# Performance work log

Measured on AMD Instinct MI355X. Metric: run time of the kernel, lower is better.

Reference implementation:

```python
import jax, jax.numpy as jnp
import numpy as np

B, S, D = 4, 4096, 512      # batch, seq_len, data_embedding_size
FH = 2048                    # forecasting_hidden_size
H = 64                       # lstm_hidden_size (proj_size=1 since H>1)


def setup_inputs() -> dict:
    key = jax.random.key(0)
    ks = jax.random.split(key, 10)
    sD, sFH, sH = 1.0 / np.sqrt(D), 1.0 / np.sqrt(FH), 1.0 / np.sqrt(H)
    return {
        "x": jax.random.normal(ks[0], (B, S, D), dtype=jnp.float32),
        # forecasting head: Linear(D->FH) then Linear(FH->D)
        "W1": jax.random.uniform(ks[1], (FH, D), minval=-sD, maxval=sD),
        "b1": jax.random.uniform(ks[2], (FH,), minval=-sD, maxval=sD),
        "W2": jax.random.uniform(ks[3], (D, FH), minval=-sFH, maxval=sFH),
        "b2": jax.random.uniform(ks[4], (D,), minval=-sFH, maxval=sFH),
        # LSTM (1 layer, proj_size=1): gate order i,f,g,o
        "Wih": jax.random.uniform(ks[5], (4 * H, D), minval=-sH, maxval=sH),
        "Whh": jax.random.uniform(ks[6], (4 * H, 1), minval=-sH, maxval=sH),  # recurrent input is projected h (size 1)
        "bih": jax.random.uniform(ks[7], (4 * H,), minval=-sH, maxval=sH),
        "bhh": jax.random.uniform(ks[8], (4 * H,), minval=-sH, maxval=sH),
        "Whr": jax.random.uniform(ks[9], (1, H), minval=-sH, maxval=sH),  # projection h_inner -> h
    }


def reference(x, W1, b1, W2, b2, Wih, Whh, bih, bhh, Whr):
    Bx, Sx, Dx = x.shape
    flat = x.reshape(-1, Dx)                       # [B*S, D]
    fore = (flat @ W1.T + b1) @ W2.T + b2          # [B*S, D]  (two linears, no activation)

    # Original code loops i in range(S) over the FLATTENED sequence -> only first S tokens.
    xs = flat[:Sx]
    fs = fore[:Sx]

    def cell(h, c, inp):
        # gates = W_ih x + b_ih + W_hh h + b_hh ; PyTorch order i,f,g,o
        g = Wih @ inp + bih + Whh @ h + bhh        # [4H]
        i, f, gg, o = jnp.split(g, 4)
        c2 = jax.nn.sigmoid(f) * c + jax.nn.sigmoid(i) * jnp.tanh(gg)
        h2 = Whr @ (jax.nn.sigmoid(o) * jnp.tanh(c2))   # projected hidden, shape [1]
        return h2, c2

    def step(carry, tok):
        h, c = carry
        xt, ft = tok
        h2, c2 = cell(h, c, xt)        # real token: updates state
        hf, _ = cell(h2, c2, ft)       # forecasted token: peeks, does not update state
        return (h2, c2), (h2[0], hf[0])

    init = (jnp.zeros((1,), x.dtype), jnp.zeros((H,), x.dtype))
    _, (p, pf) = jax.lax.scan(step, init, (xs, fs))   # p, pf: [S]

    progress = jnp.broadcast_to(p[None, :], (Bx, Sx))
    forecasted_progress = jnp.broadcast_to(pf[None, :], (Bx, Sx))
    return progress, forecasted_progress, fore.reshape(1, -1, Dx)
```

## Files before the change

### kernel.cpp

```cpp
#include <hip/hip_runtime.h>
#include <hip/hip_bf16.h>


#if __has_builtin(__builtin_amdgcn_exp2f)
__device__ __forceinline__ float EXP2(float x) { return __builtin_amdgcn_exp2f(x); }
#else
__device__ __forceinline__ float EXP2(float x) { return __expf(x * 0.6931471805599453f); }
#endif
#if __has_builtin(__builtin_amdgcn_rcpf)
__device__ __forceinline__ float RCPF(float x) { return __builtin_amdgcn_rcpf(x); }
#else
__device__ __forceinline__ float RCPF(float x) { return 1.0f / x; }
#endif

constexpr float L2E  = 1.4426950408889634f;
constexpr float L2E2 = 2.8853900817779268f;

__device__ __forceinline__ float sig_f(float x)  { return RCPF(1.0f + EXP2(-L2E * x)); }
__device__ __forceinline__ float tanh_f(float x) { return fmaf(-2.0f, RCPF(1.0f + EXP2(L2E2 * x)), 1.0f); }

template<int CTRL>
__device__ __forceinline__ float dppadd(float x) {
    return x + __int_as_float(__builtin_amdgcn_update_dpp(
        0, __float_as_int(x), CTRL, 0xf, 0xf, true));
}
__device__ __forceinline__ float dpp_sum64_lane63(float x) {
    x = dppadd<0x111>(x); x = dppadd<0x112>(x); x = dppadd<0x114>(x);
    x = dppadd<0x118>(x); x = dppadd<0x142>(x); x = dppadd<0x143>(x);
    return x;
}
__device__ __forceinline__ float readlane63(float x) {
    return __int_as_float(__builtin_amdgcn_readlane(__float_as_int(x), 63));
}
__device__ __forceinline__ float readlane_s(float x, int s) {
    return __int_as_float(__builtin_amdgcn_readlane(__float_as_int(x), s));
}

using bf16x8 = __attribute__((ext_vector_type(8))) __bf16;
using f32x4  = __attribute__((ext_vector_type(4))) float;

__device__ __forceinline__ void mfma_tile128_lds(
    const __hip_bfloat16* __restrict__ A, int lda,
    const __hip_bfloat16* __restrict__ B, int ldb,
    int K, int bm, int bn,
    const float* __restrict__ bias,
    float* __restrict__ Cf, int ldc,
    __hip_bfloat16* __restrict__ Cb,
    __hip_bfloat16* __restrict__ Ct, int ldt,
    __hip_bfloat16* __restrict__ Bs)
{
    const int tid  = threadIdx.x;
    const int w    = tid >> 6;
    const int lane = tid & 63;
    const int rc   = lane & 15;
    const int kg   = lane >> 4;
    const __hip_bfloat16* ap0 = A + (size_t)(bm + w * 16 + rc) * lda + kg * 8;
    const __hip_bfloat16* ap1 = ap0 + (size_t)64 * lda;

#define LD8(P) (*reinterpret_cast<const bf16x8*>(P))
    const f32x4 z{0.f, 0.f, 0.f, 0.f};
    f32x4 c00 = z, c01 = z, c02 = z, c03 = z;
    f32x4 c10 = z, c11 = z, c12 = z, c13 = z;

    for (int kb = 0; kb < K; kb += 512) {
        __syncthreads();
        #pragma unroll
        for (int i = 0; i < 16; ++i) {
            const int G = i * 256 + tid;
            const int row = G >> 6, kc = G & 63;
            const bf16x8 v = LD8(B + (size_t)(bn + row) * ldb + kb + kc * 8);
            *reinterpret_cast<bf16x8*>(Bs + row * 512 + ((kc ^ (row & 7)) << 3)) = v;
        }
        __syncthreads();

        bf16x8 a0 = LD8(ap0 + kb), a1 = LD8(ap1 + kb);
        #pragma unroll 4
        for (int s = 0; s < 16; ++s) {
            bf16x8 a0n = a0, a1n = a1;
            if (s < 15) {
                a0n = LD8(ap0 + kb + (s + 1) * 32);
                a1n = LD8(ap1 + kb + (s + 1) * 32);
            }
            bf16x8 bf[4];
            #pragma unroll
            for (int g = 0; g < 4; ++g) {
                const int row = g * 16 + rc;
                const int off = row * 512 + (((s * 4 + kg) ^ (row & 7)) << 3);
                bf[g] = *reinterpret_cast<const bf16x8*>(Bs + off);
            }
            c00 = __builtin_amdgcn_mfma_f32_16x16x32_bf16(a0, bf[0], c00, 0, 0, 0);
            c01 = __builtin_amdgcn_mfma_f32_16x16x32_bf16(a0, bf[1], c01, 0, 0, 0);
            c02 = __builtin_amdgcn_mfma_f32_16x16x32_bf16(a0, bf[2], c02, 0, 0, 0);
            c03 = __builtin_amdgcn_mfma_f32_16x16x32_bf16(a0, bf[3], c03, 0, 0, 0);
            c10 = __builtin_amdgcn_mfma_f32_16x16x32_bf16(a1, bf[0], c10, 0, 0, 0);
            c11 = __builtin_amdgcn_mfma_f32_16x16x32_bf16(a1, bf[1], c11, 0, 0, 0);
            c12 = __builtin_amdgcn_mfma_f32_16x16x32_bf16(a1, bf[2], c12, 0, 0, 0);
            c13 = __builtin_amdgcn_mfma_f32_16x16x32_bf16(a1, bf[3], c13, 0, 0, 0);
            a0 = a0n; a1 = a1n;
        }
    }
#undef LD8

    const int row0 = bm + w * 16 + kg * 4;
    const int colb = bn + rc;
#define EPI(ACC, HOFF, CT) {                                                  \
        const int col = colb + (CT) * 16;                                     \
        const float bb = bias ? bias[col] : 0.0f;                             \
        _Pragma("unroll")                                                     \
        for (int i = 0; i < 4; ++i) {                                         \
            const float v = (ACC)[i] + bb;                                    \
            const int row = row0 + (HOFF) + i;                                \
            if (Cf) Cf[(size_t)row * ldc + col] = v;                          \
            if (Cb) Cb[(size_t)row * ldc + col] = __float2bfloat16(v);        \
            if (Ct) Ct[(size_t)col * ldt + row] = __float2bfloat16(v);        \
        }}
    EPI(c00, 0, 0)  EPI(c01, 0, 1)  EPI(c02, 0, 2)  EPI(c03, 0, 3)
    EPI(c10, 64, 0) EPI(c11, 64, 1) EPI(c12, 64, 2) EPI(c13, 64, 3)
#undef EPI
}

__global__ __launch_bounds__(256) void conv_kernel(
    const float* __restrict__ x, const float* __restrict__ W2,
    const float* __restrict__ W1, const float* __restrict__ Wih,
    const float* __restrict__ bih, const float* __restrict__ bhh,
    __hip_bfloat16* __restrict__ xb, __hip_bfloat16* __restrict__ W2b,
    __hip_bfloat16* __restrict__ Wihb, __hip_bfloat16* __restrict__ W1t,
    float* __restrict__ gxbias)
{
    const int bid = blockIdx.x, tid = threadIdx.x;
#define CVT4(SRC, DST, BASE) {                                                \
        const size_t i = ((size_t)(BASE) * 256 + tid) * 4;                    \
        const float4 v = *reinterpret_cast<const float4*>((SRC) + i);         \
        __hip_bfloat16 o[4] = {__float2bfloat16(v.x), __float2bfloat16(v.y),  \
                               __float2bfloat16(v.z), __float2bfloat16(v.w)}; \
        *reinterpret_cast<ushort4*>((DST) + i) =                              \
            *reinterpret_cast<const ushort4*>(o); }
    if (bid < 8192) {
        CVT4(x, xb, bid)
    } else if (bid < 9216) {
        CVT4(W2, W2b, bid - 8192)
    } else if (bid < 9344) {
        CVT4(Wih, Wihb, bid - 9216)
    } else if (bid < 9600) {
        __shared__ float lds[64][65];
        const int b = bid - 9344;
        const int br = b >> 3, bc = b & 7;
        const int r0 = tid >> 4, c4 = (tid & 15) * 4;
        #pragma unroll
        for (int u = 0; u < 4; ++u) {
            const int row = r0 + u * 16;
            const float4 v = *reinterpret_cast<const float4*>(
                &W1[(size_t)(br * 64 + row) * 512 + bc * 64 + c4]);
            lds[row][c4 + 0] = v.x; lds[row][c4 + 1] = v.y;
            lds[row][c4 + 2] = v.z; lds[row][c4 + 3] = v.w;
        }
        __syncthreads();
        const int jj0 = tid >> 4, kk4 = (tid & 15) * 4;
        #pragma unroll
        for (int u = 0; u < 4; ++u) {
            const int jj = jj0 + u * 16;
            __hip_bfloat16 o[4] = {
                __float2bfloat16(lds[kk4 + 0][jj]), __float2bfloat16(lds[kk4 + 1][jj]),
                __float2bfloat16(lds[kk4 + 2][jj]), __float2bfloat16(lds[kk4 + 3][jj])};
            *reinterpret_cast<ushort4*>(
                &W1t[(size_t)(bc * 64 + jj) * 2048 + br * 64 + kk4]) =
                *reinterpret_cast<const ushort4*>(o);
        }
    } else {
        gxbias[tid] = bih[tid] + bhh[tid];
    }
#undef CVT4
}

__global__ __launch_bounds__(256) void prep_kernel(
    const float* __restrict__ W2, const float* __restrict__ b1,
    const float* __restrict__ b2,
    const __hip_bfloat16* __restrict__ W2b, const __hip_bfloat16* __restrict__ W1t,
    const __hip_bfloat16* __restrict__ xb, const __hip_bfloat16* __restrict__ Wihb,
    const float* __restrict__ gxbias,
    __hip_bfloat16* __restrict__ Weffb, __hip_bfloat16* __restrict__ WeffTb,
    float* __restrict__ beff, float* __restrict__ Gx)
{
    __shared__ __hip_bfloat16 Bs[64 * 512];
    const int bid = blockIdx.x;
    if (bid < 32) {
        const int bm = (bid >> 3) * 128, bn = (bid & 7) * 64;
        mfma_tile128_lds(W2b, 2048, W1t, 2048, 2048, bm, bn, nullptr,
                         nullptr, 512, Weffb, WeffTb, 512, Bs);
    } else if (bid < 40) {
        const int w = threadIdx.x >> 6, j = threadIdx.x & 63;
        const int base = (bid - 32) * 64 + w * 16;
        for (int o = 0; o < 16; ++o) {
            const int i = base + o;
            float s = 0.0f;
            #pragma unroll
            for (int m = 0; m < 32; ++m)
                s = fmaf(W2[(size_t)i * 2048 + j + 64 * m], b1[j + 64 * m], s);
            s = dpp_sum64_lane63(s);
            if (j == 63) beff[i] = s + b2[i];
        }
    } else {
        const int b = bid - 40;
        const int bm = (b >> 2) * 128, bn = (b & 3) * 64;
        mfma_tile128_lds(xb, 512, Wihb, 512, 512, bm, bn, gxbias,
                         Gx, 256, nullptr, nullptr, 0, Bs);
    }
}

__global__ __launch_bounds__(256) void fused_kernel(
    int phase, int first, int last,
    int fore_cnt, int gf_cnt, int wg_cnt,
    const __hip_bfloat16* __restrict__ xb, const __hip_bfloat16* __restrict__ Weffb,
    const __hip_bfloat16* __restrict__ WeffTb, const __hip_bfloat16* __restrict__ Wihb,
    __hip_bfloat16* __restrict__ Wgb, const __hip_bfloat16* __restrict__ Wgb_in,
    const float* __restrict__ Wih, const float* __restrict__ beff,
    float* __restrict__ bf2_out, const float* __restrict__ bf2,
    const float* __restrict__ Gx, float* __restrict__ Gf,
    const float* __restrict__ Gf_in, const float* __restrict__ gxbias,
    const float* __restrict__ Whh, const float* __restrict__ Whr,
    const float* __restrict__ hprev, float* __restrict__ hnext,
    float* __restrict__ P, float* __restrict__ Q,
    float* __restrict__ fore, float* __restrict__ out)
{
    __shared__ __hip_bfloat16 Bs[64 * 512];
    constexpr int CH = 32;
    constexpr int S = 4096, BS = 4 * 4096;

    if (blockIdx.x < 32) {
        const int chunk = blockIdx.x * 4 + (threadIdx.x >> 6);
        const int j = threadIdx.x & 63;
        const float wi = Whh[j], wf = Whh[64 + j];
        const float wg2 = Whh[128 + j], wo = Whh[192 + j];
        const float* ab = Gx + (size_t)chunk * CH * 256 + j;

        float hp = 0.0f;
        if (!first) {
            const int idx = chunk * CH - 1 + j;
            hp = (idx >= 0 && idx < S) ? hprev[idx] : 0.0f;
        }

        if (phase == 0) {
            float Pv = 1.0f, Qv = 0.0f;
            #pragma unroll 8
            for (int s = 0; s < CH; ++s) {
                const float hs = first ? 0.0f : readlane_s(hp, s);
                const float ai = ab[s * 256]       + wi  * hs;
                const float af = ab[s * 256 + 64]  + wf  * hs;
                const float ag = ab[s * 256 + 128] + wg2 * hs;
                const float si = sig_f(ai);
                const float sf = sig_f(af);
                const float tg = tanh_f(ag);
                Pv = sf * Pv;
                Qv = fmaf(sf, Qv, si * tg);
            }
            P[chunk * 64 + j] = Pv;
            Q[chunk * 64 + j] = Qv;
        } else {
            const float whr = Whr[j];
            float c = 0.0f;
            #pragma unroll 8
            for (int m = 0; m < chunk; ++m)
                c = fmaf(P[m * 64 + j], c, Q[m * 64 + j]);
            float vp = 0.0f, vpf = 0.0f;
            const float* gfp = Gf_in ? Gf_in + (size_t)chunk * CH * 256 + j : nullptr;
            const float bi0 = gxbias[j],        bi1 = gxbias[64 + j];
            const float bi2 = gxbias[128 + j],  bi3 = gxbias[192 + j];
            #pragma unroll 4
            for (int s = 0; s < CH; ++s) {
                const float hs = first ? 0.0f : readlane_s(hp, s);
                const float ai = ab[s * 256]       + wi  * hs;
                const float af = ab[s * 256 + 64]  + wf  * hs;
                const float ag = ab[s * 256 + 128] + wg2 * hs;
                const float ao = ab[s * 256 + 192] + wo  * hs;
                const float si = sig_f(ai);
                const float sf = sig_f(af);
                const float tg = tanh_f(ag);
                const float so = sig_f(ao);
                c = fmaf(sf, c, si * tg);
                const float tc = tanh_f(c);
                float hv = tc * (so * whr);
                hv = dpp_sum64_lane63(hv);
                const float hn = readlane63(hv);
                vp = (j == s) ? hn : vp;
                if (last) {
                    const float fi = gfp[s * 256]       + bi0 + wi  * hn;
                    const float ff = gfp[s * 256 + 64]  + bi1 + wf  * hn;
                    const float fg = gfp[s * 256 + 128] + bi2 + wg2 * hn;
                    const float fo = gfp[s * 256 + 192] + bi3 + wo  * hn;
                    const float cf = sig_f(ff) * c + sig_f(fi) * tanh_f(fg);
                    float hf = sig_f(fo) * tanh_f(cf) * whr;
                    hf = dpp_sum64_lane63(hf);
                    const float hfn = readlane63(hf);
                    vpf = (j == s) ? hfn : vpf;
                }
            }
            if (j < CH) {
                const int t = chunk * CH + j;
                if (last) {
                    #pragma unroll
                    for (int b = 0; b < 4; ++b) {
                        out[b * S + t]      = vp;
                        out[BS + b * S + t] = vpf;
                    }
                } else {
                    hnext[t] = vp;
                }
            }
        }
        return;
    }

    const int bt = blockIdx.x - 32;
    if (bt < fore_cnt) {
        const int bm = (bt >> 3) * 128, bn = (bt & 7) * 64;
        mfma_tile128_lds(xb, 512, Weffb, 512, 512, bm, bn, beff,
                         fore, 512, nullptr, nullptr, 0, Bs);
    } else if (bt < fore_cnt + gf_cnt) {
        const int g = bt - fore_cnt;
        const int bm = (g >> 2) * 128, bn = (g & 3) * 64;
        mfma_tile128_lds(xb, 512, Wgb_in, 512, 512, bm, bn, bf2,
                         Gf, 256, nullptr, nullptr, 0, Bs);
    } else if (bt < fore_cnt + gf_cnt + wg_cnt) {
        const int t = bt - fore_cnt - gf_cnt;
        if (t < 16) {
            const int bm = (t >> 3) * 128, bn = (t & 7) * 64;
            mfma_tile128_lds(Wihb, 512, WeffTb, 512, 512, bm, bn, nullptr,
                             nullptr, 512, Wgb, nullptr, 0, Bs);
        } else {
            const int w = threadIdx.x >> 6, j = threadIdx.x & 63;
            for (int o = 0; o < 64; ++o) {
                const int i = w * 64 + o;
                float s = 0.0f;
                #pragma unroll
                for (int m = 0; m < 8; ++m)
                    s = fmaf(Wih[(size_t)i * 512 + j + 64 * m], beff[j + 64 * m], s);
                s = dpp_sum64_lane63(s);
                if (j == 63) bf2_out[i] = s;
            }
        }
    }
}

extern "C" void kernel_launch(void* const* d_in, const int* in_sizes, int n_in,
                              void* d_out, int out_size, void* d_ws, size_t ws_size,
                              hipStream_t stream) {
    const float* x   = (const float*)d_in[0];
    const float* W1  = (const float*)d_in[1];
    const float* b1  = (const float*)d_in[2];
    const float* W2  = (const float*)d_in[3];
    const float* b2  = (const float*)d_in[4];
    const float* Wih = (const float*)d_in[5];
    const float* Whh = (const float*)d_in[6];
    const float* bih = (const float*)d_in[7];
    const float* bhh = (const float*)d_in[8];
    const float* Whr = (const float*)d_in[9];
    float* out = (float*)d_out;

    constexpr int Bb = 4, S = 4096;
    const int M = Bb * S;

    float* ws      = (float*)d_ws;
    float* beff    = ws;
    float* gxbias  = beff + 512;
    float* bf2     = gxbias + 256;
    float* Gx      = bf2 + 256;
    float* Gf      = Gx + S * 256;
    float* Pp      = Gf + S * 256;
    float* Qq      = Pp + 8192;
    float* h0      = Qq + 8192;
    float* h1      = h0 + S;
    __hip_bfloat16* xb     = (__hip_bfloat16*)(h1 + S);
    __hip_bfloat16* W2b    = xb + (size_t)M * 512;
    __hip_bfloat16* W1t    = W2b + 512 * 2048;
    __hip_bfloat16* Wihb   = W1t + 512 * 2048;
    __hip_bfloat16* Weffb  = Wihb + 256 * 512;
    __hip_bfloat16* WeffTb = Weffb + 512 * 512;
    __hip_bfloat16* Wgb    = WeffTb + 512 * 512;

    float* fore = out + 2 * M;

    conv_kernel<<<9601, 256, 0, stream>>>(
        x, W2, W1, Wih, bih, bhh, xb, W2b, Wihb, W1t, gxbias);

    prep_kernel<<<168, 256, 0, stream>>>(
        W2, b1, b2, W2b, W1t, xb, Wihb, gxbias, Weffb, WeffTb, beff, Gx);

    fused_kernel<<<32 + 1024 + 17, 256, 0, stream>>>(
        0, 1, 0, 1024, 0, 17,
        xb, Weffb, WeffTb, Wihb, Wgb, Wgb, Wih, beff, bf2, bf2,
        Gx, Gf, nullptr, gxbias, Whh, Whr,
        h0, h0, Pp, Qq, fore, out);

    fused_kernel<<<32 + 128, 256, 0, stream>>>(
        1, 1, 0, 0, 128, 0,
        xb, Weffb, WeffTb, Wihb, Wgb, Wgb, Wih, beff, bf2, bf2,
        Gx, Gf, nullptr, gxbias, Whh, Whr,
        h0, h0, Pp, Qq, fore, out);

    fused_kernel<<<32, 256, 0, stream>>>(
        0, 0, 0, 0, 0, 0,
        xb, Weffb, WeffTb, Wihb, Wgb, Wgb, Wih, beff, bf2, bf2,
        Gx, Gf, nullptr, gxbias, Whh, Whr,
        h0, h1, Pp, Qq, fore, out);

    fused_kernel<<<32, 256, 0, stream>>>(
        1, 0, 1, 0, 0, 0,
        xb, Weffb, WeffTb, Wihb, Wgb, Wgb, Wih, beff, bf2, bf2,
        Gx, Gf, Gf, gxbias, Whh, Whr,
        h0, h1, Pp, Qq, fore, out);
}
```

Baseline: 154.7 us.

## Reschedule prep stages: overlap x conversion with Weff GEMM, split Wg/Gx kernel

```diff
diff --git a/kernel.cpp b/kernel.cpp
--- a/kernel.cpp
+++ b/kernel.cpp
@@ -119,13 +119,12 @@
 #undef EPI
 }
 
-__global__ __launch_bounds__(256) void conv_kernel(
-    const float* __restrict__ x, const float* __restrict__ W2,
-    const float* __restrict__ W1, const float* __restrict__ Wih,
+__global__ __launch_bounds__(256) void convA_kernel(
+    const float* __restrict__ W2, const float* __restrict__ W1,
+    const float* __restrict__ Wih,
     const float* __restrict__ bih, const float* __restrict__ bhh,
-    __hip_bfloat16* __restrict__ xb, __hip_bfloat16* __restrict__ W2b,
-    __hip_bfloat16* __restrict__ Wihb, __hip_bfloat16* __restrict__ W1t,
-    float* __restrict__ gxbias)
+    __hip_bfloat16* __restrict__ W2b, __hip_bfloat16* __restrict__ W1t,
+    __hip_bfloat16* __restrict__ Wihb, float* __restrict__ gxbias)
 {
     const int bid = blockIdx.x, tid = threadIdx.x;
 #define CVT4(SRC, DST, BASE) {                                                \
@@ -135,15 +134,11 @@
                                __float2bfloat16(v.z), __float2bfloat16(v.w)}; \
         *reinterpret_cast<ushort4*>((DST) + i) =                              \
             *reinterpret_cast<const ushort4*>(o); }
-    if (bid < 8192) {
-        CVT4(x, xb, bid)
-    } else if (bid < 9216) {
-        CVT4(W2, W2b, bid - 8192)
-    } else if (bid < 9344) {
-        CVT4(Wih, Wihb, bid - 9216)
-    } else if (bid < 9600) {
+    if (bid < 1024) {
+        CVT4(W2, W2b, bid)
+    } else if (bid < 1280) {
         __shared__ float lds[64][65];
-        const int b = bid - 9344;
+        const int b = bid - 1024;
         const int br = b >> 3, bc = b & 7;
         const int r0 = tid >> 4, c4 = (tid & 15) * 4;
         #pragma unroll
@@ -166,29 +161,30 @@
                 &W1t[(size_t)(bc * 64 + jj) * 2048 + br * 64 + kk4]) =
                 *reinterpret_cast<const ushort4*>(o);
         }
+    } else if (bid < 1408) {
+        CVT4(Wih, Wihb, bid - 1280)
     } else {
         gxbias[tid] = bih[tid] + bhh[tid];
     }
 #undef CVT4
 }
 
-__global__ __launch_bounds__(256) void prep_kernel(
-    const float* __restrict__ W2, const float* __restrict__ b1,
-    const float* __restrict__ b2,
+__global__ __launch_bounds__(256) void convB_kernel(
+    const float* __restrict__ x, const float* __restrict__ W2,
+    const float* __restrict__ b1, const float* __restrict__ b2,
     const __hip_bfloat16* __restrict__ W2b, const __hip_bfloat16* __restrict__ W1t,
-    const __hip_bfloat16* __restrict__ xb, const __hip_bfloat16* __restrict__ Wihb,
-    const float* __restrict__ gxbias,
+    __hip_bfloat16* __restrict__ xb,
     __hip_bfloat16* __restrict__ Weffb, __hip_bfloat16* __restrict__ WeffTb,
-    float* __restrict__ beff, float* __restrict__ Gx)
+    float* __restrict__ beff)
 {
     __shared__ __hip_bfloat16 Bs[64 * 512];
-    const int bid = blockIdx.x;
+    const int bid = blockIdx.x, tid = threadIdx.x;
     if (bid < 32) {
         const int bm = (bid >> 3) * 128, bn = (bid & 7) * 64;
         mfma_tile128_lds(W2b, 2048, W1t, 2048, 2048, bm, bn, nullptr,
                          nullptr, 512, Weffb, WeffTb, 512, Bs);
     } else if (bid < 40) {
-        const int w = threadIdx.x >> 6, j = threadIdx.x & 63;
+        const int w = tid >> 6, j = tid & 63;
         const int base = (bid - 32) * 64 + w * 16;
         for (int o = 0; o < 16; ++o) {
             const int i = base + o;
@@ -201,6 +197,47 @@
         }
     } else {
         const int b = bid - 40;
+        const float4* src = reinterpret_cast<const float4*>(x) + (size_t)b * 1024;
+        ushort4* dst = reinterpret_cast<ushort4*>(xb) + (size_t)b * 1024;
+        float4 v[4];
+        #pragma unroll
+        for (int u = 0; u < 4; ++u) v[u] = src[u * 256 + tid];
+        #pragma unroll
+        for (int u = 0; u < 4; ++u) {
+            __hip_bfloat16 o[4] = {__float2bfloat16(v[u].x), __float2bfloat16(v[u].y),
+                                   __float2bfloat16(v[u].z), __float2bfloat16(v[u].w)};
+            dst[u * 256 + tid] = *reinterpret_cast<const ushort4*>(o);
+        }
+    }
+}
+
+__global__ __launch_bounds__(256) void wggx_kernel(
+    const __hip_bfloat16* __restrict__ Wihb, const __hip_bfloat16* __restrict__ WeffTb,
+    const __hip_bfloat16* __restrict__ xb,
+    const float* __restrict__ Wih, const float* __restrict__ beff,
+    const float* __restrict__ gxbias,
+    __hip_bfloat16* __restrict__ Wgb, float* __restrict__ bf2,
+    float* __restrict__ Gx)
+{
+    __shared__ __hip_bfloat16 Bs[64 * 512];
+    const int bid = blockIdx.x;
+    if (bid < 16) {
+        const int bm = (bid >> 3) * 128, bn = (bid & 7) * 64;
+        mfma_tile128_lds(Wihb, 512, WeffTb, 512, 512, bm, bn, nullptr,
+                         nullptr, 512, Wgb, nullptr, 0, Bs);
+    } else if (bid == 16) {
+        const int w = threadIdx.x >> 6, j = threadIdx.x & 63;
+        for (int o = 0; o < 64; ++o) {
+            const int i = w * 64 + o;
+            float s = 0.0f;
+            #pragma unroll
+            for (int m = 0; m < 8; ++m)
+                s = fmaf(Wih[(size_t)i * 512 + j + 64 * m], beff[j + 64 * m], s);
+            s = dpp_sum64_lane63(s);
+            if (j == 63) bf2[i] = s;
+        }
+    } else {
+        const int b = bid - 17;
         const int bm = (b >> 2) * 128, bn = (b & 3) * 64;
         mfma_tile128_lds(xb, 512, Wihb, 512, 512, bm, bn, gxbias,
                          Gx, 256, nullptr, nullptr, 0, Bs);
@@ -209,12 +246,10 @@
 
 __global__ __launch_bounds__(256) void fused_kernel(
     int phase, int first, int last,
-    int fore_cnt, int gf_cnt, int wg_cnt,
+    int fore_cnt, int gf_cnt,
     const __hip_bfloat16* __restrict__ xb, const __hip_bfloat16* __restrict__ Weffb,
-    const __hip_bfloat16* __restrict__ WeffTb, const __hip_bfloat16* __restrict__ Wihb,
-    __hip_bfloat16* __restrict__ Wgb, const __hip_bfloat16* __restrict__ Wgb_in,
-    const float* __restrict__ Wih, const float* __restrict__ beff,
-    float* __restrict__ bf2_out, const float* __restrict__ bf2,
+    const __hip_bfloat16* __restrict__ Wgb_in,
+    const float* __restrict__ beff, const float* __restrict__ bf2,
     const float* __restrict__ Gx, float* __restrict__ Gf,
     const float* __restrict__ Gf_in, const float* __restrict__ gxbias,
     const float* __restrict__ Whh, const float* __restrict__ Whr,
@@ -312,7 +347,8 @@
 
     const int bt = blockIdx.x - 32;
     if (bt < fore_cnt) {
-        const int bm = (bt >> 3) * 128, bn = (bt & 7) * 64;
+        const int tile = (bt & 7) * 128 + (bt >> 3);
+        const int bm = (tile >> 3) * 128, bn = (tile & 7) * 64;
         mfma_tile128_lds(xb, 512, Weffb, 512, 512, bm, bn, beff,
                          fore, 512, nullptr, nullptr, 0, Bs);
     } else if (bt < fore_cnt + gf_cnt) {
@@ -320,24 +356,6 @@
         const int bm = (g >> 2) * 128, bn = (g & 3) * 64;
         mfma_tile128_lds(xb, 512, Wgb_in, 512, 512, bm, bn, bf2,
                          Gf, 256, nullptr, nullptr, 0, Bs);
-    } else if (bt < fore_cnt + gf_cnt + wg_cnt) {
-        const int t = bt - fore_cnt - gf_cnt;
-        if (t < 16) {
-            const int bm = (t >> 3) * 128, bn = (t & 7) * 64;
-            mfma_tile128_lds(Wihb, 512, WeffTb, 512, 512, bm, bn, nullptr,
-                             nullptr, 512, Wgb, nullptr, 0, Bs);
-        } else {
-            const int w = threadIdx.x >> 6, j = threadIdx.x & 63;
-            for (int o = 0; o < 64; ++o) {
-                const int i = w * 64 + o;
-                float s = 0.0f;
-                #pragma unroll
-                for (int m = 0; m < 8; ++m)
-                    s = fmaf(Wih[(size_t)i * 512 + j + 64 * m], beff[j + 64 * m], s);
-                s = dpp_sum64_lane63(s);
-                if (j == 63) bf2_out[i] = s;
-            }
-        }
     }
 }
 
@@ -379,33 +397,32 @@
 
     float* fore = out + 2 * M;
 
-    conv_kernel<<<9601, 256, 0, stream>>>(
-        x, W2, W1, Wih, bih, bhh, xb, W2b, Wihb, W1t, gxbias);
-
-    prep_kernel<<<168, 256, 0, stream>>>(
-        W2, b1, b2, W2b, W1t, xb, Wihb, gxbias, Weffb, WeffTb, beff, Gx);
-
-    fused_kernel<<<32 + 1024 + 17, 256, 0, stream>>>(
-        0, 1, 0, 1024, 0, 17,
-        xb, Weffb, WeffTb, Wihb, Wgb, Wgb, Wih, beff, bf2, bf2,
-        Gx, Gf, nullptr, gxbias, Whh, Whr,
+    convA_kernel<<<1409, 256, 0, stream>>>(
+        W2, W1, Wih, bih, bhh, W2b, W1t, Wihb, gxbias);
+
+    convB_kernel<<<2088, 256, 0, stream>>>(
+        x, W2, b1, b2, W2b, W1t, xb, Weffb, WeffTb, beff);
+
+    wggx_kernel<<<145, 256, 0, stream>>>(
+        Wihb, WeffTb, xb, Wih, beff, gxbias, Wgb, bf2, Gx);
+
+    fused_kernel<<<32 + 1024, 256, 0, stream>>>(
+        0, 1, 0, 1024, 0,
+        xb, Weffb, Wgb, beff, bf2, Gx, Gf, nullptr, gxbias, Whh, Whr,
         h0, h0, Pp, Qq, fore, out);
 
     fused_kernel<<<32 + 128, 256, 0, stream>>>(
-        1, 1, 0, 0, 128, 0,
-        xb, Weffb, WeffTb, Wihb, Wgb, Wgb, Wih, beff, bf2, bf2,
-        Gx, Gf, nullptr, gxbias, Whh, Whr,
+        1, 1, 0, 0, 128,
+        xb, Weffb, Wgb, beff, bf2, Gx, Gf, nullptr, gxbias, Whh, Whr,
         h0, h0, Pp, Qq, fore, out);
 
     fused_kernel<<<32, 256, 0, stream>>>(
-        0, 0, 0, 0, 0, 0,
-        xb, Weffb, WeffTb, Wihb, Wgb, Wgb, Wih, beff, bf2, bf2,
-        Gx, Gf, nullptr, gxbias, Whh, Whr,
+        0, 0, 0, 0, 0,
+        xb, Weffb, Wgb, beff, bf2, Gx, Gf, nullptr, gxbias, Whh, Whr,
         h0, h1, Pp, Qq, fore, out);
 
     fused_kernel<<<32, 256, 0, stream>>>(
-        1, 0, 1, 0, 0, 0,
-        xb, Weffb, WeffTb, Wihb, Wgb, Wgb, Wih, beff, bf2, bf2,
-        Gx, Gf, Gf, gxbias, Whh, Whr,
+        1, 0, 1, 0, 0,
+        xb, Weffb, Wgb, beff, bf2, Gx, Gf, Gf, gxbias, Whh, Whr,
         h0, h1, Pp, Qq, fore, out);
 }
```

Result: no change. 152.2 us (-1.6%).
